# Kernel tuning notes

Measured on AMD Instinct MI355X. Metric: run time of the kernel, lower is better.

The kernel has to match this reference:

```python
import jax, jax.numpy as jnp
import numpy as np

D_MODEL = 1024
N_HEADS = 16
D_HEAD = D_MODEL // N_HEADS


def setup_inputs() -> dict:
    key = jax.random.key(0)
    k1, k2, k3, k4, k5, k6 = jax.random.split(key, 6)
    B, Q, T = 4, 1024, 4096
    s = 1.0 / np.sqrt(D_MODEL)  # ~ kaiming-uniform scale for Linear weights
    return {
        "q_in": jax.random.normal(k1, (B, Q, D_MODEL), dtype=jnp.float32),
        "kv_in": jax.random.normal(k2, (B, T, D_MODEL), dtype=jnp.float32),
        "Wq": jax.random.normal(k3, (D_MODEL, D_MODEL), dtype=jnp.float32) * s,
        "Wk": jax.random.normal(k4, (D_MODEL, D_MODEL), dtype=jnp.float32) * s,
        "Wv": jax.random.normal(k5, (D_MODEL, D_MODEL), dtype=jnp.float32) * s,
        "Wo": jax.random.normal(k6, (D_MODEL, D_MODEL), dtype=jnp.float32) * s,
    }


def reference(q_in, kv_in, Wq, Wk, Wv, Wo):
    B, Q, D = q_in.shape
    T = kv_in.shape[1]
    scale = D_HEAD ** -0.5
    # projections; torch Linear: y = x @ W.T
    q = (q_in @ Wq.T).reshape(B, Q, N_HEADS, D_HEAD)
    k = (kv_in @ Wk.T).reshape(B, T, N_HEADS, D_HEAD)
    v = (kv_in @ Wv.T).reshape(B, T, N_HEADS, D_HEAD)
    # scores [B, H, Q, T]
    w = jnp.einsum("bqhd,bthd->bhqt", q, k) * scale
    w = jax.nn.softmax(w.astype(jnp.float32), axis=-1).astype(q.dtype)
    # dropout p=0.0 -> identity
    out = jnp.einsum("bhqt,bthd->bqhd", w, v).reshape(B, Q, D)
    return out @ Wo.T
```

## Files before the change

### kernel.cpp

```cpp
#include <hip/hip_runtime.h>
#include <hip/hip_bf16.h>
#include <cstdint>
#include <cstddef>

#define DM 1024
#define NH 16
#define DH 64
#define BQ 1024
#define TT 4096
#define BB 4
#define NSPLIT 4
#define TSPLIT (TT / NSPLIT)

using f32x4 = __attribute__((ext_vector_type(4))) float;
using f32x16 = __attribute__((ext_vector_type(16))) float;
using s16x8 = __attribute__((ext_vector_type(8))) short;

__device__ __forceinline__ unsigned short f2bf(float f) {
  union { __hip_bfloat16 h; unsigned short u; } c;
  c.h = __float2bfloat16(f);
  return c.u;
}

__device__ __forceinline__ float exp2_raw(float x) {
  return __builtin_amdgcn_exp2f(x);
}

__device__ __forceinline__ f32x16 zero16() {
  f32x16 z;
#pragma unroll
  for (int i = 0; i < 16; i++) z[i] = 0.f;
  return z;
}

__device__ __forceinline__ int cvtpk(float lo, float hi2) {
  int r;
  asm("v_cvt_pk_bf16_f32 %0, %1, %2" : "=v"(r) : "v"(lo), "v"(hi2));
  return r;
}

template<int RB>
__device__ __forceinline__ s16x8 mkfrag(const f32x16& p, int hi) {
  const int W1 = cvtpk(p[RB + 0], p[RB + 1]);
  const int W3 = cvtpk(p[RB + 2], p[RB + 3]);
  const int W2 = cvtpk(p[RB + 4], p[RB + 5]);
  const int W4 = cvtpk(p[RB + 6], p[RB + 7]);
  const int s1 = __shfl_xor(W1, 32);
  const int s3 = __shfl_xor(W3, 32);
  const int s2 = __shfl_xor(W2, 32);
  const int s4 = __shfl_xor(W4, 32);
  union { int i[4]; s16x8 v; } u;
  u.i[0] = hi ? s2 : W1;
  u.i[1] = hi ? s4 : W3;
  u.i[2] = hi ? W2 : s1;
  u.i[3] = hi ? W4 : s3;
  return u.v;
}

__global__ void cvt_f32_bf16(const float* __restrict__ in, unsigned short* __restrict__ out, int n4) {
  int i = blockIdx.x * blockDim.x + threadIdx.x;
  if (i < n4) {
    float4 v = reinterpret_cast<const float4*>(in)[i];
    ushort4 o;
    o.x = f2bf(v.x); o.y = f2bf(v.y); o.z = f2bf(v.z); o.w = f2bf(v.w);
    reinterpret_cast<ushort4*>(out)[i] = o;
  }
}

__global__ void cvt_w4(const float* __restrict__ w0, const float* __restrict__ w1,
                       const float* __restrict__ w2, const float* __restrict__ w3,
                       unsigned short* __restrict__ o0, unsigned short* __restrict__ o1,
                       unsigned short* __restrict__ o2, unsigned short* __restrict__ o3,
                       int n4) {
  int i = blockIdx.x * blockDim.x + threadIdx.x;
  if (i >= n4) return;
  const float* in; unsigned short* out;
  switch (blockIdx.y) {
    case 0: in = w0; out = o0; break;
    case 1: in = w1; out = o1; break;
    case 2: in = w2; out = o2; break;
    default: in = w3; out = o3; break;
  }
  float4 v = reinterpret_cast<const float4*>(in)[i];
  ushort4 o;
  o.x = f2bf(v.x); o.y = f2bf(v.y); o.z = f2bf(v.z); o.w = f2bf(v.w);
  reinterpret_cast<ushort4*>(out)[i] = o;
}

__device__ __forceinline__ void gload_lds16(const unsigned short* g, unsigned short* l) {
  __builtin_amdgcn_global_load_lds(
      (const __attribute__((address_space(1))) unsigned int*)g,
      (__attribute__((address_space(3))) unsigned int*)l,
      16, 0, 0);
}

template<int MODE, int SEQ, bool PRESCALE>
__global__ __launch_bounds__(256) void gemm_bt(const unsigned short* __restrict__ A,
                                               const unsigned short* __restrict__ W,
                                               unsigned short* __restrict__ Cb,
                                               float* __restrict__ Cf) {
  __shared__ unsigned short As[128 * 32];
  __shared__ unsigned short Bs[128 * 32];
  const int tid = threadIdx.x;
  const int wid = tid >> 6, lane = tid & 63;
  const int m0 = blockIdx.x * 128, n0 = blockIdx.y * 128;
  const int wr = wid >> 1, wc = wid & 1;
  const int fr = lane & 15;
  const int fk = (lane >> 4) * 8;

  f32x4 acc[4][4];
#pragma unroll
  for (int mt = 0; mt < 4; mt++)
#pragma unroll
    for (int nt = 0; nt < 4; nt++) acc[mt][nt] = f32x4{0.f, 0.f, 0.f, 0.f};

  const unsigned short* gA = A + (size_t)(m0 + wid * 32 + (lane >> 2)) * DM + (lane & 3) * 8;
  const unsigned short* gW = W + (size_t)(n0 + wid * 32 + (lane >> 2)) * DM + (lane & 3) * 8;
  unsigned short* lA0 = &As[(wid * 32) * 32];
  unsigned short* lA1 = &As[(wid * 32 + 16) * 32];
  unsigned short* lB0 = &Bs[(wid * 32) * 32];
  unsigned short* lB1 = &Bs[(wid * 32 + 16) * 32];

  for (int kt = 0; kt < DM / 32; ++kt) {
    gload_lds16(gA, lA0);
    gload_lds16(gA + 16 * DM, lA1);
    gload_lds16(gW, lB0);
    gload_lds16(gW + 16 * DM, lB1);
    gA += 32; gW += 32;
    __syncthreads();
    s16x8 af[4], bfv[4];
#pragma unroll
    for (int mt = 0; mt < 4; mt++)
      af[mt] = *reinterpret_cast<const s16x8*>(&As[(wr * 64 + mt * 16 + fr) * 32 + fk]);
#pragma unroll
    for (int nt = 0; nt < 4; nt++)
      bfv[nt] = *reinterpret_cast<const s16x8*>(&Bs[(wc * 64 + nt * 16 + fr) * 32 + fk]);
    __builtin_amdgcn_s_setprio(1);
#pragma unroll
    for (int mt = 0; mt < 4; mt++)
#pragma unroll
      for (int nt = 0; nt < 4; nt++)
        acc[mt][nt] = __builtin_amdgcn_mfma_f32_16x16x32_bf16(af[mt], bfv[nt], acc[mt][nt], 0, 0, 0);
    __builtin_amdgcn_s_setprio(0);
    __syncthreads();
  }

#pragma unroll
  for (int mt = 0; mt < 4; mt++) {
#pragma unroll
    for (int nt = 0; nt < 4; nt++) {
      const int col = n0 + wc * 64 + nt * 16 + fr;
#pragma unroll
      for (int r = 0; r < 4; r++) {
        const int m = m0 + wr * 64 + mt * 16 + (lane >> 4) * 4 + r;
        float v = acc[mt][nt][r];
        if constexpr (PRESCALE) v *= 0.18033688011112042f;
        if constexpr (MODE == 0) {
          const int b = m / SEQ, sr = m % SEQ;
          const int h = col >> 6, dh = col & 63;
          Cb[((size_t)(b * NH + h) * SEQ + sr) * DH + dh] = f2bf(v);
        } else {
          Cf[(size_t)m * DM + col] = v;
        }
      }
    }
  }
}

__global__ __launch_bounds__(256) void gemm_kv(const unsigned short* __restrict__ A,
                                               const unsigned short* __restrict__ Wkv,
                                               unsigned short* __restrict__ Kp,
                                               unsigned short* __restrict__ Vt) {
  __shared__ unsigned short As[128 * 32];
  __shared__ unsigned short Bs[128 * 32];
  const int tid = threadIdx.x;
  const int wid = tid >> 6, lane = tid & 63;
  const int m0 = blockIdx.x * 128, n0 = blockIdx.y * 128;
  const int wr = wid >> 1, wc = wid & 1;
  const int fr = lane & 15;
  const int fk = (lane >> 4) * 8;

  f32x4 acc[4][4];
#pragma unroll
  for (int mt = 0; mt < 4; mt++)
#pragma unroll
    for (int nt = 0; nt < 4; nt++) acc[mt][nt] = f32x4{0.f, 0.f, 0.f, 0.f};

  const unsigned short* gA = A + (size_t)(m0 + wid * 32 + (lane >> 2)) * DM + (lane & 3) * 8;
  const unsigned short* gW = Wkv + (size_t)(n0 + wid * 32 + (lane >> 2)) * DM + (lane & 3) * 8;
  unsigned short* lA0 = &As[(wid * 32) * 32];
  unsigned short* lA1 = &As[(wid * 32 + 16) * 32];
  unsigned short* lB0 = &Bs[(wid * 32) * 32];
  unsigned short* lB1 = &Bs[(wid * 32 + 16) * 32];

  for (int kt = 0; kt < DM / 32; ++kt) {
    gload_lds16(gA, lA0);
    gload_lds16(gA + 16 * DM, lA1);
    gload_lds16(gW, lB0);
    gload_lds16(gW + 16 * DM, lB1);
    gA += 32; gW += 32;
    __syncthreads();
    s16x8 af[4], bfv[4];
#pragma unroll
    for (int mt = 0; mt < 4; mt++)
      af[mt] = *reinterpret_cast<const s16x8*>(&As[(wr * 64 + mt * 16 + fr) * 32 + fk]);
#pragma unroll
    for (int nt = 0; nt < 4; nt++)
      bfv[nt] = *reinterpret_cast<const s16x8*>(&Bs[(wc * 64 + nt * 16 + fr) * 32 + fk]);
    __builtin_amdgcn_s_setprio(1);
#pragma unroll
    for (int mt = 0; mt < 4; mt++)
#pragma unroll
      for (int nt = 0; nt < 4; nt++)
        acc[mt][nt] = __builtin_amdgcn_mfma_f32_16x16x32_bf16(af[mt], bfv[nt], acc[mt][nt], 0, 0, 0);
    __builtin_amdgcn_s_setprio(0);
    __syncthreads();
  }

  const int klg = lane >> 4;
#pragma unroll
  for (int mt = 0; mt < 4; mt++) {
#pragma unroll
    for (int nt = 0; nt < 4; nt++) {
      const int col = n0 + wc * 64 + nt * 16 + fr;
      const int tb = m0 + wr * 64 + mt * 16 + klg * 4;
      const int b = tb >> 12, sr = tb & (TT - 1);
      if (col < DM) {
        const int h = col >> 6, dh = col & 63;
#pragma unroll
        for (int r = 0; r < 4; r++)
          Kp[((size_t)(b * NH + h) * TT + sr + r) * DH + dh] = f2bf(acc[mt][nt][r]);
      } else {
        const int c2 = col - DM;
        const int h = c2 >> 6, dh = c2 & 63;
        ushort4 pk;
        pk.x = f2bf(acc[mt][nt][0]);
        pk.y = f2bf(acc[mt][nt][1]);
        pk.z = f2bf(acc[mt][nt][2]);
        pk.w = f2bf(acc[mt][nt][3]);
        *reinterpret_cast<ushort4*>(&Vt[((size_t)(b * NH + h) * DH + dh) * TT + sr]) = pk;
      }
    }
  }
}

__global__ __launch_bounds__(512) void attn_kern(const unsigned short* __restrict__ Qp,
                                                 const unsigned short* __restrict__ Kp,
                                                 const unsigned short* __restrict__ Vtg,
                                                 float* __restrict__ Opart,
                                                 float2* __restrict__ ml) {
  __shared__ unsigned short Ks[2][64 * 64];
  __shared__ unsigned short Vs[2][64 * 64];
  __shared__ float als[8][32];
  const int bh = blockIdx.x;
  const int q0 = blockIdx.y * 256;
  const int split = blockIdx.z;
  const int t00 = split * TSPLIT;
  const int tid = threadIdx.x, wid = tid >> 6, lane = tid & 63;
  const int l31 = lane & 31, hi = lane >> 5;

  const size_t qrow = (size_t)bh * BQ + q0 + wid * 32 + l31;
  s16x8 qf[4];
#pragma unroll
  for (int kk = 0; kk < 4; kk++)
    qf[kk] = *reinterpret_cast<const s16x8*>(&Qp[qrow * DH + 16 * kk + 8 * hi]);

  f32x16 o0 = zero16(), o1 = zero16();
  float mrun = -3e38f, lsum = 0.f;

  const size_t kvbase = (size_t)bh * TT * DH;
  const int rk = tid >> 3;
  const int c8 = tid & 7;

  auto stage = [&](int buf, int t0) {
    gload_lds16(Kp + kvbase + (size_t)(t0 + rk) * DH + (c8 ^ (rk & 7)) * 8,
                &Ks[buf][wid * 512]);
    gload_lds16(Vtg + kvbase + (size_t)rk * TT + t0 + (c8 ^ (rk & 7)) * 8,
                &Vs[buf][wid * 512]);
  };

  stage(0, t00);
  __syncthreads();

  const int rowA = l31;
  const int rowB = 32 + l31;
  const int sw = l31 & 7;

  for (int it = 0; it < TSPLIT / 64; ++it) {
    const int cur = it & 1;
    if (it + 1 < TSPLIT / 64) stage(cur ^ 1, t00 + (it + 1) * 64);

    f32x16 s0 = zero16(), s1 = zero16();
    __builtin_amdgcn_s_setprio(1);
#pragma unroll
    for (int kk = 0; kk < 4; kk++) {
      s16x8 kb0 = *reinterpret_cast<const s16x8*>(&Ks[cur][rowA * 64 + (((2 * kk + hi) ^ sw) * 8)]);
      s0 = __builtin_amdgcn_mfma_f32_32x32x16_bf16(kb0, qf[kk], s0, 0, 0, 0);
      s16x8 kb1 = *reinterpret_cast<const s16x8*>(&Ks[cur][rowB * 64 + (((2 * kk + hi) ^ sw) * 8)]);
      s1 = __builtin_amdgcn_mfma_f32_32x32x16_bf16(kb1, qf[kk], s1, 0, 0, 0);
    }
    __builtin_amdgcn_s_setprio(0);

    float tm = fmaxf(s0[0], s1[0]);
#pragma unroll
    for (int r = 1; r < 16; r++) tm = fmaxf(tm, fmaxf(s0[r], s1[r]));
    tm = fmaxf(tm, __shfl_xor(tm, 32));

    if (__any(tm - mrun > 8.f)) {
      const float mn = fmaxf(mrun, tm);
      const float al = exp2_raw(mrun - mn);
      mrun = mn;
      lsum *= al;
      if (lane < 32) als[wid][lane] = al;
#pragma unroll
      for (int r = 0; r < 16; r++) {
        const float av = als[wid][(r & 3) + 8 * (r >> 2) + 4 * hi];
        o0[r] *= av; o1[r] *= av;
      }
    }

#pragma unroll
    for (int r = 0; r < 16; r++) {
      s0[r] = exp2_raw(s0[r] - mrun); lsum += s0[r];
      s1[r] = exp2_raw(s1[r] - mrun); lsum += s1[r];
    }

    s16x8 pa[4];
    pa[0] = mkfrag<0>(s0, hi);
    pa[1] = mkfrag<8>(s0, hi);
    pa[2] = mkfrag<0>(s1, hi);
    pa[3] = mkfrag<8>(s1, hi);

    __builtin_amdgcn_s_setprio(1);
#pragma unroll
    for (int kk = 0; kk < 4; kk++) {
      s16x8 vb0 = *reinterpret_cast<const s16x8*>(&Vs[cur][rowA * 64 + (((2 * kk + hi) ^ sw) * 8)]);
      o0 = __builtin_amdgcn_mfma_f32_32x32x16_bf16(pa[kk], vb0, o0, 0, 0, 0);
      s16x8 vb1 = *reinterpret_cast<const s16x8*>(&Vs[cur][rowB * 64 + (((2 * kk + hi) ^ sw) * 8)]);
      o1 = __builtin_amdgcn_mfma_f32_32x32x16_bf16(pa[kk], vb1, o1, 0, 0, 0);
    }
    __builtin_amdgcn_s_setprio(0);

    __syncthreads();
  }

  lsum += __shfl_xor(lsum, 32);
  if (lane < 32)
    ml[((size_t)split * (BB * NH) + bh) * BQ + q0 + wid * 32 + lane] = float2{mrun, lsum};

#pragma unroll
  for (int r = 0; r < 16; r++) {
    const int q = (r & 3) + 8 * (r >> 2) + 4 * hi;
    const size_t orow = (((size_t)split * (BB * NH) + bh) * BQ + q0 + wid * 32 + q) * DH;
    Opart[orow + l31] = o0[r];
    Opart[orow + 32 + l31] = o1[r];
  }
}

__global__ __launch_bounds__(256) void attn_combine(const float* __restrict__ Opart,
                                                    const float2* __restrict__ ml,
                                                    unsigned short* __restrict__ Ob) {
  const int gid = blockIdx.x * 256 + threadIdx.x;
  const int row = gid >> 4, seg = gid & 15;
  float2 a[NSPLIT];
#pragma unroll
  for (int s = 0; s < NSPLIT; s++) a[s] = ml[(size_t)s * (BB * NH * BQ) + row];
  float m = a[0].x;
#pragma unroll
  for (int s = 1; s < NSPLIT; s++) m = fmaxf(m, a[s].x);
  float w[NSPLIT], denom = 0.f;
#pragma unroll
  for (int s = 0; s < NSPLIT; s++) { w[s] = exp2_raw(a[s].x - m); denom += a[s].y * w[s]; }
  const float inv = 1.0f / denom;
  float4 acc = {0.f, 0.f, 0.f, 0.f};
#pragma unroll
  for (int s = 0; s < NSPLIT; s++) {
    const float4 p = reinterpret_cast<const float4*>(Opart)[(size_t)s * (BB * NH * BQ) * 16 + (size_t)row * 16 + seg];
    acc.x += p.x * w[s]; acc.y += p.y * w[s]; acc.z += p.z * w[s]; acc.w += p.w * w[s];
  }
  const int bh = row >> 10, q = row & (BQ - 1);
  const int b = bh >> 4, h = bh & 15;
  ushort4 o;
  o.x = f2bf(acc.x * inv);
  o.y = f2bf(acc.y * inv);
  o.z = f2bf(acc.z * inv);
  o.w = f2bf(acc.w * inv);
  *reinterpret_cast<ushort4*>(&Ob[((size_t)b * BQ + q) * DM + h * DH + seg * 4]) = o;
}

extern "C" void kernel_launch(void* const* d_in, const int* in_sizes, int n_in,
                              void* d_out, int out_size, void* d_ws, size_t ws_size,
                              hipStream_t stream) {
  const float* q_in = (const float*)d_in[0];
  const float* kv_in = (const float*)d_in[1];
  const float* Wq = (const float*)d_in[2];
  const float* Wk = (const float*)d_in[3];
  const float* Wv = (const float*)d_in[4];
  const float* Wo = (const float*)d_in[5];
  float* out = (float*)d_out;

  char* ws = (char*)d_ws;
  unsigned short* qin_b = (unsigned short*)ws;  ws += (size_t)BB * BQ * DM * 2;
  unsigned short* kvin_b = (unsigned short*)ws; ws += (size_t)BB * TT * DM * 2;
  unsigned short* Wq_b = (unsigned short*)ws;   ws += (size_t)DM * DM * 2;
  unsigned short* Wk_b = (unsigned short*)ws;   ws += (size_t)DM * DM * 2;
  unsigned short* Wv_b = (unsigned short*)ws;   ws += (size_t)DM * DM * 2;
  unsigned short* Wo_b = (unsigned short*)ws;   ws += (size_t)DM * DM * 2;
  unsigned short* qp = (unsigned short*)ws;     ws += (size_t)BB * NH * BQ * DH * 2;
  unsigned short* kp = (unsigned short*)ws;     ws += (size_t)BB * NH * TT * DH * 2;
  unsigned short* vt = (unsigned short*)ws;     ws += (size_t)BB * NH * DH * TT * 2;
  unsigned short* ao = (unsigned short*)ws;     ws += (size_t)BB * BQ * DM * 2;
  float* Opart = (float*)ws;                    ws += (size_t)NSPLIT * BB * NH * BQ * DH * 4;
  float2* mlb = (float2*)ws;                    ws += (size_t)NSPLIT * BB * NH * BQ * 8;

  const int qn4 = BB * BQ * DM / 4;
  const int kvn4 = BB * TT * DM / 4;
  const int wn4 = DM * DM / 4;
  cvt_f32_bf16<<<(qn4 + 255) / 256, 256, 0, stream>>>(q_in, qin_b, qn4);
  cvt_f32_bf16<<<(kvn4 + 255) / 256, 256, 0, stream>>>(kv_in, kvin_b, kvn4);
  cvt_w4<<<dim3((wn4 + 255) / 256, 4), 256, 0, stream>>>(Wq, Wk, Wv, Wo,
                                                         Wq_b, Wk_b, Wv_b, Wo_b, wn4);

  dim3 blk(256);
  gemm_bt<0, BQ, true><<<dim3(BB * BQ / 128, DM / 128), blk, 0, stream>>>(qin_b, Wq_b, qp, nullptr);
  gemm_kv<<<dim3(BB * TT / 128, 2 * DM / 128), blk, 0, stream>>>(kvin_b, Wk_b, kp, vt);

  attn_kern<<<dim3(BB * NH, BQ / 256, NSPLIT), dim3(512), 0, stream>>>(qp, kp, vt, Opart, mlb);
  attn_combine<<<dim3(BB * NH * BQ * 16 / 256), blk, 0, stream>>>(Opart, mlb, ao);

  gemm_bt<1, BQ, false><<<dim3(BB * BQ / 128, DM / 128), blk, 0, stream>>>(ao, Wo_b, nullptr, out);
}
```

Measured before the change: 282.7 us.

## Add XCD-aware block swizzle to GEMMs, halve attention splits, unroll attention loop

The projection GEMMs now launch a flattened 1D grid and remap block indices so that consecutive tiles land on the same XCD. This is meant to improve L2 reuse of the A and W tiles. The attention kernel reduces the KV split count from 4 to 2, which shrinks the partial-output traffic and the combine work, at the cost of fewer blocks in flight. The attention loop is also unrolled by two with a fixed double-buffer schedule and precomputed LDS byte offsets, and it adds a min-blocks-per-CU launch bound hint.

```diff
diff --git a/kernel.cpp b/kernel.cpp
--- a/kernel.cpp
+++ b/kernel.cpp
@@ -9,7 +9,7 @@
 #define BQ 1024
 #define TT 4096
 #define BB 4
-#define NSPLIT 4
+#define NSPLIT 2
 #define TSPLIT (TT / NSPLIT)
 
 using f32x4 = __attribute__((ext_vector_type(4))) float;
@@ -94,7 +94,11 @@
       16, 0, 0);
 }
 
-template<int MODE, int SEQ, bool PRESCALE>
+__device__ __forceinline__ int xcd_swz(int lin, int nwg) {
+  return (lin & 7) * (nwg >> 3) + (lin >> 3);
+}
+
+template<int MODE, int SEQ, bool PRESCALE, int NT>
 __global__ __launch_bounds__(256) void gemm_bt(const unsigned short* __restrict__ A,
                                                const unsigned short* __restrict__ W,
                                                unsigned short* __restrict__ Cb,
@@ -103,7 +107,8 @@
   __shared__ unsigned short Bs[128 * 32];
   const int tid = threadIdx.x;
   const int wid = tid >> 6, lane = tid & 63;
-  const int m0 = blockIdx.x * 128, n0 = blockIdx.y * 128;
+  const int swz = xcd_swz(blockIdx.x, gridDim.x);
+  const int m0 = (swz / NT) * 128, n0 = (swz % NT) * 128;
   const int wr = wid >> 1, wc = wid & 1;
   const int fr = lane & 15;
   const int fk = (lane >> 4) * 8;
@@ -175,7 +180,8 @@
   __shared__ unsigned short Bs[128 * 32];
   const int tid = threadIdx.x;
   const int wid = tid >> 6, lane = tid & 63;
-  const int m0 = blockIdx.x * 128, n0 = blockIdx.y * 128;
+  const int swz = xcd_swz(blockIdx.x, gridDim.x);
+  const int m0 = (swz >> 4) * 128, n0 = (swz & 15) * 128;
   const int wr = wid >> 1, wc = wid & 1;
   const int fr = lane & 15;
   const int fk = (lane >> 4) * 8;
@@ -244,13 +250,67 @@
   }
 }
 
-__global__ __launch_bounds__(512) void attn_kern(const unsigned short* __restrict__ Qp,
-                                                 const unsigned short* __restrict__ Kp,
-                                                 const unsigned short* __restrict__ Vtg,
-                                                 float* __restrict__ Opart,
-                                                 float2* __restrict__ ml) {
-  __shared__ unsigned short Ks[2][64 * 64];
-  __shared__ unsigned short Vs[2][64 * 64];
+#define ATTN_TILE(CUR, DO_STAGE, SBUF)                                             \
+  do {                                                                             \
+    if (DO_STAGE) {                                                                \
+      gload_lds16(gK, &KVs[(SBUF)][wid * 512]);                                    \
+      gload_lds16(gV, &KVs[2 + (SBUF)][wid * 512]);                                \
+      gK += 64 * DH; gV += 64;                                                     \
+    }                                                                              \
+    f32x16 s0 = zero16(), s1 = zero16();                                           \
+    __builtin_amdgcn_s_setprio(1);                                                 \
+    _Pragma("unroll")                                                              \
+    for (int kk = 0; kk < 4; kk++) {                                               \
+      s16x8 kb0 = *reinterpret_cast<const s16x8*>(lds0 + (CUR) * 8192 + offA[kk]); \
+      s0 = __builtin_amdgcn_mfma_f32_32x32x16_bf16(kb0, qf[kk], s0, 0, 0, 0);      \
+      s16x8 kb1 = *reinterpret_cast<const s16x8*>(lds0 + (CUR) * 8192 + offB[kk]); \
+      s1 = __builtin_amdgcn_mfma_f32_32x32x16_bf16(kb1, qf[kk], s1, 0, 0, 0);      \
+    }                                                                              \
+    __builtin_amdgcn_s_setprio(0);                                                 \
+    float tm = fmaxf(s0[0], s1[0]);                                                \
+    _Pragma("unroll")                                                              \
+    for (int r = 1; r < 16; r++) tm = fmaxf(tm, fmaxf(s0[r], s1[r]));              \
+    tm = fmaxf(tm, __shfl_xor(tm, 32));                                            \
+    if (__any(tm - mrun > 8.f)) {                                                  \
+      const float mn = fmaxf(mrun, tm);                                            \
+      const float al = exp2_raw(mrun - mn);                                        \
+      mrun = mn;                                                                   \
+      lsum *= al;                                                                  \
+      if (lane < 32) als[wid][lane] = al;                                          \
+      _Pragma("unroll")                                                            \
+      for (int r = 0; r < 16; r++) {                                               \
+        const float av = als[wid][(r & 3) + 8 * (r >> 2) + 4 * hi];                \
+        o0[r] *= av; o1[r] *= av;                                                  \
+      }                                                                            \
+    }                                                                              \
+    _Pragma("unroll")                                                              \
+    for (int r = 0; r < 16; r++) {                                                 \
+      s0[r] = exp2_raw(s0[r] - mrun); lsum += s0[r];                               \
+      s1[r] = exp2_raw(s1[r] - mrun); lsum += s1[r];                               \
+    }                                                                              \
+    s16x8 pa[4];                                                                   \
+    pa[0] = mkfrag<0>(s0, hi);                                                     \
+    pa[1] = mkfrag<8>(s0, hi);                                                     \
+    pa[2] = mkfrag<0>(s1, hi);                                                     \
+    pa[3] = mkfrag<8>(s1, hi);                                                     \
+    __builtin_amdgcn_s_setprio(1);                                                 \
+    _Pragma("unroll")                                                              \
+    for (int kk = 0; kk < 4; kk++) {                                               \
+      s16x8 vb0 = *reinterpret_cast<const s16x8*>(lds0 + 16384 + (CUR) * 8192 + offA[kk]); \
+      o0 = __builtin_amdgcn_mfma_f32_32x32x16_bf16(pa[kk], vb0, o0, 0, 0, 0);      \
+      s16x8 vb1 = *reinterpret_cast<const s16x8*>(lds0 + 16384 + (CUR) * 8192 + offB[kk]); \
+      o1 = __builtin_amdgcn_mfma_f32_32x32x16_bf16(pa[kk], vb1, o1, 0, 0, 0);      \
+    }                                                                              \
+    __builtin_amdgcn_s_setprio(0);                                                 \
+    __syncthreads();                                                               \
+  } while (0)
+
+__global__ __launch_bounds__(512, 4) void attn_kern(const unsigned short* __restrict__ Qp,
+                                                    const unsigned short* __restrict__ Kp,
+                                                    const unsigned short* __restrict__ Vtg,
+                                                    float* __restrict__ Opart,
+                                                    float2* __restrict__ ml) {
+  __shared__ unsigned short KVs[4][64 * 64];
   __shared__ float als[8][32];
   const int bh = blockIdx.x;
   const int q0 = blockIdx.y * 256;
@@ -272,76 +332,27 @@
   const int rk = tid >> 3;
   const int c8 = tid & 7;
 
-  auto stage = [&](int buf, int t0) {
-    gload_lds16(Kp + kvbase + (size_t)(t0 + rk) * DH + (c8 ^ (rk & 7)) * 8,
-                &Ks[buf][wid * 512]);
-    gload_lds16(Vtg + kvbase + (size_t)rk * TT + t0 + (c8 ^ (rk & 7)) * 8,
-                &Vs[buf][wid * 512]);
-  };
-
-  stage(0, t00);
+  const unsigned short* gK = Kp + kvbase + (size_t)(t00 + rk) * DH + (c8 ^ (rk & 7)) * 8;
+  const unsigned short* gV = Vtg + kvbase + (size_t)rk * TT + t00 + (c8 ^ (rk & 7)) * 8;
+
+  const char* lds0 = (const char*)&KVs[0][0];
+  const int sw = l31 & 7;
+  int offA[4], offB[4];
+#pragma unroll
+  for (int kk = 0; kk < 4; kk++) {
+    offA[kk] = (l31 * 64 + (((2 * kk + hi) ^ sw) * 8)) * 2;
+    offB[kk] = ((32 + l31) * 64 + (((2 * kk + hi) ^ sw) * 8)) * 2;
+  }
+
+  gload_lds16(gK, &KVs[0][wid * 512]);
+  gload_lds16(gV, &KVs[2][wid * 512]);
+  gK += 64 * DH; gV += 64;
   __syncthreads();
 
-  const int rowA = l31;
-  const int rowB = 32 + l31;
-  const int sw = l31 & 7;
-
-  for (int it = 0; it < TSPLIT / 64; ++it) {
-    const int cur = it & 1;
-    if (it + 1 < TSPLIT / 64) stage(cur ^ 1, t00 + (it + 1) * 64);
-
-    f32x16 s0 = zero16(), s1 = zero16();
-    __builtin_amdgcn_s_setprio(1);
-#pragma unroll
-    for (int kk = 0; kk < 4; kk++) {
-      s16x8 kb0 = *reinterpret_cast<const s16x8*>(&Ks[cur][rowA * 64 + (((2 * kk + hi) ^ sw) * 8)]);
-      s0 = __builtin_amdgcn_mfma_f32_32x32x16_bf16(kb0, qf[kk], s0, 0, 0, 0);
-      s16x8 kb1 = *reinterpret_cast<const s16x8*>(&Ks[cur][rowB * 64 + (((2 * kk + hi) ^ sw) * 8)]);
-      s1 = __builtin_amdgcn_mfma_f32_32x32x16_bf16(kb1, qf[kk], s1, 0, 0, 0);
-    }
-    __builtin_amdgcn_s_setprio(0);
-
-    float tm = fmaxf(s0[0], s1[0]);
-#pragma unroll
-    for (int r = 1; r < 16; r++) tm = fmaxf(tm, fmaxf(s0[r], s1[r]));
-    tm = fmaxf(tm, __shfl_xor(tm, 32));
-
-    if (__any(tm - mrun > 8.f)) {
-      const float mn = fmaxf(mrun, tm);
-      const float al = exp2_raw(mrun - mn);
-      mrun = mn;
-      lsum *= al;
-      if (lane < 32) als[wid][lane] = al;
-#pragma unroll
-      for (int r = 0; r < 16; r++) {
-        const float av = als[wid][(r & 3) + 8 * (r >> 2) + 4 * hi];
-        o0[r] *= av; o1[r] *= av;
-      }
-    }
-
-#pragma unroll
-    for (int r = 0; r < 16; r++) {
-      s0[r] = exp2_raw(s0[r] - mrun); lsum += s0[r];
-      s1[r] = exp2_raw(s1[r] - mrun); lsum += s1[r];
-    }
-
-    s16x8 pa[4];
-    pa[0] = mkfrag<0>(s0, hi);
-    pa[1] = mkfrag<8>(s0, hi);
-    pa[2] = mkfrag<0>(s1, hi);
-    pa[3] = mkfrag<8>(s1, hi);
-
-    __builtin_amdgcn_s_setprio(1);
-#pragma unroll
-    for (int kk = 0; kk < 4; kk++) {
-      s16x8 vb0 = *reinterpret_cast<const s16x8*>(&Vs[cur][rowA * 64 + (((2 * kk + hi) ^ sw) * 8)]);
-      o0 = __builtin_amdgcn_mfma_f32_32x32x16_bf16(pa[kk], vb0, o0, 0, 0, 0);
-      s16x8 vb1 = *reinterpret_cast<const s16x8*>(&Vs[cur][rowB * 64 + (((2 * kk + hi) ^ sw) * 8)]);
-      o1 = __builtin_amdgcn_mfma_f32_32x32x16_bf16(pa[kk], vb1, o1, 0, 0, 0);
-    }
-    __builtin_amdgcn_s_setprio(0);
-
-    __syncthreads();
+  const int NIT = TSPLIT / 128;
+  for (int it2 = 0; it2 < NIT; ++it2) {
+    ATTN_TILE(0, true, 1);
+    ATTN_TILE(1, (it2 < NIT - 1), 0);
   }
 
   lsum += __shfl_xor(lsum, 32);
@@ -422,11 +433,11 @@
                                                          Wq_b, Wk_b, Wv_b, Wo_b, wn4);
 
   dim3 blk(256);
-  gemm_bt<0, BQ, true><<<dim3(BB * BQ / 128, DM / 128), blk, 0, stream>>>(qin_b, Wq_b, qp, nullptr);
-  gemm_kv<<<dim3(BB * TT / 128, 2 * DM / 128), blk, 0, stream>>>(kvin_b, Wk_b, kp, vt);
+  gemm_bt<0, BQ, true, 8><<<dim3(BB * BQ / 128 * 8), blk, 0, stream>>>(qin_b, Wq_b, qp, nullptr);
+  gemm_kv<<<dim3(BB * TT / 128 * 16), blk, 0, stream>>>(kvin_b, Wk_b, kp, vt);
 
   attn_kern<<<dim3(BB * NH, BQ / 256, NSPLIT), dim3(512), 0, stream>>>(qp, kp, vt, Opart, mlb);
   attn_combine<<<dim3(BB * NH * BQ * 16 / 256), blk, 0, stream>>>(Opart, mlb, ao);
 
-  gemm_bt<1, BQ, false><<<dim3(BB * BQ / 128, DM / 128), blk, 0, stream>>>(ao, Wo_b, nullptr, out);
-}
+  gemm_bt<1, BQ, false, 8><<<dim3(BB * BQ / 128 * 8), blk, 0, stream>>>(ao, Wo_b, nullptr, out);
+}
```

After: 270.5 us. 4.3% less time.
